# Kernel optimization log

Hardware: AMD Instinct MI355X
Metric: run time of the kernel (lower is better)

Reference implementation:

```python
import jax, jax.numpy as jnp
import numpy as np

C_REG = 0.1
MAX_ITER = 15
FEAT_SCALE = 0.05  # keep linear-kernel entries O(1) for a well-conditioned QP


def batched_kronecker(a, b):
    # a: (B,n,m), b: (B,p,q) -> (B, n*p, m*q); matches torch batched_kronecker
    B, n, m = a.shape
    _, p, q = b.shape
    return jnp.einsum('bij,bkl->bikjl', a, b).reshape(B, n * p, m * q)


def solve_qp_batch(G, e, h, A, b, max_iter):
    # Solves min_z 0.5 z^T G z + e^T z  s.t.  z <= h (C = I), A z = b
    # via a primal-dual interior-point method, batched over tasks.
    # (Same QP as qpth.QPFunction with C = identity.)
    def solve_one(G, e, h, A, b):
        nz = G.shape[0]
        neq = A.shape[0]
        nineq = h.shape[0]  # == nz since C = I
        z0 = jnp.zeros(nz, G.dtype)
        nu0 = jnp.zeros(neq, G.dtype)
        s0 = jnp.ones(nineq, G.dtype)
        lam0 = jnp.ones(nineq, G.dtype)

        def step(carry, _):
            z, nu, s, lam = carry
            rd = G @ z + e + lam + A.T @ nu          # dual residual (C^T lam = lam)
            rp = z + s - h                            # primal ineq residual (C z = z)
            rp2 = A @ z - b                           # primal eq residual
            mu = jnp.dot(s, lam) / nineq
            rc = lam * s - 0.1 * mu                   # centered complementarity
            d = lam / s
            H = G + jnp.diag(d)                       # G + C^T diag(lam/s) C with C = I
            r1 = -rd + (rc - lam * rp) / s
            KKT = jnp.block([[H, A.T], [A, jnp.zeros((neq, neq), G.dtype)]])
            rhs = jnp.concatenate([r1, -rp2])
            sol = jnp.linalg.solve(KKT, rhs)
            dz = sol[:nz]
            dnu = sol[nz:]
            ds = -rp - dz
            dlam = (-rc - lam * ds) / s
            a_s = jnp.min(jnp.where(ds < 0, -s / ds, jnp.inf))
            a_l = jnp.min(jnp.where(dlam < 0, -lam / dlam, jnp.inf))
            alpha = jnp.minimum(1.0, 0.99 * jnp.minimum(a_s, a_l))
            return (z + alpha * dz, nu + alpha * dnu, s + alpha * ds, lam + alpha * dlam), None

        (z, _, _, _), _ = jax.lax.scan(step, (z0, nu0, s0, lam0), None, length=max_iter)
        return z

    return jax.vmap(solve_one)(G, e, h, A, b)


def setup_inputs() -> dict:
    key = jax.random.key(0)
    k1, k2, k3 = jax.random.split(key, 3)
    B, N, K, Q, D = 32, 10, 10, 15, 512
    support = jax.random.normal(k1, (B, N, K, D), dtype=jnp.float32) * FEAT_SCALE
    support_labels = jax.random.randint(k2, (B, N, K), 0, N)
    query = jax.random.normal(k3, (B, N, Q, D), dtype=jnp.float32) * FEAT_SCALE
    return {"support": support, "support_labels": support_labels, "query": query}


def reference(support, support_labels, query):
    B, N, K, D = support.shape
    Q = query.shape[2]
    n_way = N
    n_support = N * K
    sup = support.reshape(B, n_support, D)
    qry = query.reshape(B, N * Q, D)

    # Gram matrix and block-kronecker QP Hessian: G = K(sup,sup) kron I_nway + I
    kernel = jnp.einsum('bnd,bmd->bnm', sup, sup)
    I_way = jnp.broadcast_to(jnp.eye(n_way, dtype=sup.dtype), (B, n_way, n_way))
    G = batched_kronecker(kernel, I_way) + jnp.eye(n_way * n_support, dtype=sup.dtype)

    y = jax.nn.one_hot(support_labels.reshape(B, n_support), n_way, dtype=sup.dtype)
    y_flat = y.reshape(B, n_support * n_way)
    e = -y_flat
    h = C_REG * y_flat

    # A = I_nsupport kron ones(1, n_way): sums alphas over classes per support point
    I_sup = jnp.broadcast_to(jnp.eye(n_support, dtype=sup.dtype), (B, n_support, n_support))
    A = batched_kronecker(I_sup, jnp.ones((B, 1, n_way), dtype=sup.dtype))
    b = jnp.zeros((B, n_support), dtype=sup.dtype)

    qp_sol = solve_qp_batch(G, e, h, A, b, MAX_ITER)  # (B, n_support*n_way)

    compat = jnp.einsum('bnd,bmd->bnm', sup, qry)     # (B, n_support, n_query)
    qp_sol = qp_sol.reshape(B, n_support, n_way)
    logits = jnp.einsum('bsq,bsn->bqn', compat, qp_sol)  # (B, n_query, n_way)
    return logits
```

## Files before the change

### kernel.cpp

```cpp
#include <hip/hip_runtime.h>

constexpr int kB   = 32;
constexpr int kNS  = 100;
constexpr int kNW  = 10;
constexpr int kNZ  = 1000;
constexpr int kD   = 512;
constexpr int kNQ  = 150;
constexpr int kIt  = 15;
constexpr int kPan = 4;
constexpr int kGrp = 8;
constexpr int kRQ  = 13;
constexpr int kNSP = kGrp * kRQ;

__global__ __launch_bounds__(128) void gram_kernel(const float* __restrict__ sup,
                                                   float* __restrict__ Kf)
{
    const int i = blockIdx.x;
    const int b = blockIdx.y;
    const int tid = threadIdx.x;
    __shared__ float rowi[kD];
    const float* supb = sup + (size_t)b * kNS * kD;
    reinterpret_cast<float4*>(rowi)[tid] =
        reinterpret_cast<const float4*>(supb + (size_t)i * kD)[tid];
    __syncthreads();
    for (int j = tid; j < kNS; j += 128) {
        const float4* rj = reinterpret_cast<const float4*>(supb + (size_t)j * kD);
        float acc = 0.0f;
        for (int d4 = 0; d4 < kD / 4; ++d4) {
            float4 v = rj[d4];
            acc += rowi[4*d4+0]*v.x + rowi[4*d4+1]*v.y
                 + rowi[4*d4+2]*v.z + rowi[4*d4+3]*v.w;
        }
        Kf[((size_t)b * kNS + i) * kNS + j] = acc;
    }
}

__global__ __launch_bounds__(256) void compat_kernel(const float* __restrict__ sup,
                                                     const float* __restrict__ qry,
                                                     float* __restrict__ compat)
{
    const int i = blockIdx.x;
    const int b = blockIdx.y;
    const int tid = threadIdx.x;
    __shared__ float rowi[kD];
    const float* supb = sup + (size_t)b * kNS * kD;
    const float* qryb = qry + (size_t)b * kNQ * kD;
    if (tid < 128)
        reinterpret_cast<float4*>(rowi)[tid] =
            reinterpret_cast<const float4*>(supb + (size_t)i * kD)[tid];
    __syncthreads();
    for (int j = tid; j < kNQ; j += 256) {
        const float4* rj = reinterpret_cast<const float4*>(qryb + (size_t)j * kD);
        float acc = 0.0f;
        for (int d4 = 0; d4 < kD / 4; ++d4) {
            float4 v = rj[d4];
            acc += rowi[4*d4+0]*v.x + rowi[4*d4+1]*v.y
                 + rowi[4*d4+2]*v.z + rowi[4*d4+3]*v.w;
        }
        compat[((size_t)b * kNS + i) * kNQ + j] = acc;
    }
}

__global__ __launch_bounds__(256) void init_kernel(double* __restrict__ z,
                                                   double* __restrict__ nu,
                                                   double* __restrict__ s,
                                                   double* __restrict__ lam,
                                                   double* __restrict__ mu_g)
{
    const int b = blockIdx.x;
    const int tid = threadIdx.x;
    for (int m = tid; m < kNZ; m += 256) {
        z[b*kNZ + m]   = 0.0;
        s[b*kNZ + m]   = 1.0;
        lam[b*kNZ + m] = 1.0;
    }
    if (tid < kNS) nu[b*kNS + tid] = 0.0;
    if (tid == 0)  mu_g[b] = 1.0;
}

__device__ __forceinline__ void adj4_solvef(const float B[4][4],
                                            const float b1[4], const float b2[4],
                                            float m1[4], float m2[4])
{
    const float s0 = B[0][0]*B[1][1] - B[1][0]*B[0][1];
    const float s1 = B[0][0]*B[1][2] - B[1][0]*B[0][2];
    const float s2 = B[0][0]*B[1][3] - B[1][0]*B[0][3];
    const float s3 = B[0][1]*B[1][2] - B[1][1]*B[0][2];
    const float s4 = B[0][1]*B[1][3] - B[1][1]*B[0][3];
    const float s5 = B[0][2]*B[1][3] - B[1][2]*B[0][3];
    const float c5 = B[2][2]*B[3][3] - B[3][2]*B[2][3];
    const float c4 = B[2][1]*B[3][3] - B[3][1]*B[2][3];
    const float c3 = B[2][1]*B[3][2] - B[3][1]*B[2][2];
    const float c2 = B[2][0]*B[3][3] - B[3][0]*B[2][3];
    const float c1 = B[2][0]*B[3][2] - B[3][0]*B[2][2];
    const float c0 = B[2][0]*B[3][1] - B[3][0]*B[2][1];
    const float det = s0*c5 - s1*c4 + s2*c3 + s3*c2 - s4*c1 + s5*c0;
    const float id = 1.0f / det;
    {
        const float r0 = ( B[1][1]*c5 - B[1][2]*c4 + B[1][3]*c3) * id;
        const float r1 = (-B[0][1]*c5 + B[0][2]*c4 - B[0][3]*c3) * id;
        const float r2 = ( B[3][1]*s5 - B[3][2]*s4 + B[3][3]*s3) * id;
        const float r3 = (-B[2][1]*s5 + B[2][2]*s4 - B[2][3]*s3) * id;
        m1[0] = r0*b1[0] + r1*b1[1] + r2*b1[2] + r3*b1[3];
        m2[0] = r0*b2[0] + r1*b2[1] + r2*b2[2] + r3*b2[3];
    }
    {
        const float r0 = (-B[1][0]*c5 + B[1][2]*c2 - B[1][3]*c1) * id;
        const float r1 = ( B[0][0]*c5 - B[0][2]*c2 + B[0][3]*c1) * id;
        const float r2 = (-B[3][0]*s5 + B[3][2]*s2 - B[3][3]*s1) * id;
        const float r3 = ( B[2][0]*s5 - B[2][2]*s2 + B[2][3]*s1) * id;
        m1[1] = r0*b1[0] + r1*b1[1] + r2*b1[2] + r3*b1[3];
        m2[1] = r0*b2[0] + r1*b2[1] + r2*b2[2] + r3*b2[3];
    }
    {
        const float r0 = ( B[1][0]*c4 - B[1][1]*c2 + B[1][3]*c0) * id;
        const float r1 = (-B[0][0]*c4 + B[0][1]*c2 - B[0][3]*c0) * id;
        const float r2 = ( B[3][0]*s4 - B[3][1]*s2 + B[3][3]*s0) * id;
        const float r3 = (-B[2][0]*s4 + B[2][1]*s2 - B[2][3]*s0) * id;
        m1[2] = r0*b1[0] + r1*b1[1] + r2*b1[2] + r3*b1[3];
        m2[2] = r0*b2[0] + r1*b2[1] + r2*b2[2] + r3*b2[3];
    }
    {
        const float r0 = (-B[1][0]*c3 + B[1][1]*c1 - B[1][2]*c0) * id;
        const float r1 = ( B[0][0]*c3 - B[0][1]*c1 + B[0][2]*c0) * id;
        const float r2 = (-B[3][0]*s3 + B[3][1]*s1 - B[3][2]*s0) * id;
        const float r3 = ( B[2][0]*s3 - B[2][1]*s1 + B[2][2]*s0) * id;
        m1[3] = r0*b1[0] + r1*b1[1] + r2*b1[2] + r3*b1[3];
        m2[3] = r0*b2[0] + r1*b2[1] + r2*b2[2] + r3*b2[3];
    }
}

#define PANEL_UPDATE2F(H1, H2, WSG, BUF, BASE, SCL1, SCL2, M1, M2)            \
    {                                                                          \
        _Pragma("unroll")                                                      \
        for (int r = 0; r < kRQ; ++r) { H1[r] *= SCL1; H2[r] *= SCL2; }        \
        _Pragma("unroll")                                                      \
        for (int p = 0; p < kPan; ++p) {                                       \
            const float mp1 = M1[p], mp2 = M2[p];                              \
            float w[kRQ];                                                      \
            _Pragma("unroll")                                                  \
            for (int u = 0; u < kRQ; ++u) w[u] = WSG[BUF][p][BASE + u];        \
            __builtin_amdgcn_sched_barrier(0);                                 \
            _Pragma("unroll")                                                  \
            for (int u = 0; u < kRQ; ++u) {                                    \
                H1[u] = fmaf(-mp1, w[u], H1[u]);                               \
                H2[u] = fmaf(-mp2, w[u], H2[u]);                               \
            }                                                                  \
        }                                                                      \
    }

__global__ __launch_bounds__(512) void ipm_invert_kernel(
    const float* __restrict__ Kf, const int* __restrict__ labels,
    const double* __restrict__ z, const double* __restrict__ nu,
    const double* __restrict__ s, const double* __restrict__ lam,
    const double* __restrict__ mu_g,
    float* __restrict__ Hinv, double* __restrict__ tvec)
{
    const int b = blockIdx.x / kNW;
    const int a = blockIdx.x - b * kNW;
    const int tid = threadIdx.x;
    const int h = tid >> 6;
    const int lane = tid & 63;
    const int base = h * kRQ;
    const int j1 = lane;
    const int j2 = 64 + lane;
    const bool a2 = (j2 < kNS);
    const int js2 = a2 ? j2 : j1;

    __shared__ double za[kNS], sa[kNS], la[kNS], nus[kNS], r1s[kNS];
    __shared__ float  daf[kNS];
    __shared__ double part[kGrp][kNS];
    __shared__ alignas(16) float Wr [2][kPan][kNSP + 8];
    __shared__ alignas(16) float Wsg[2][kPan][kNSP + 8];
    __shared__ int labs[kNS];

    const double* zb = z   + (size_t)b * kNZ;
    const double* sb = s   + (size_t)b * kNZ;
    const double* lb = lam + (size_t)b * kNZ;
    const float*  Kb = Kf  + (size_t)b * kNS * kNS;

    if (tid < kNS) {
        double zv = zb[tid * kNW + a];
        double sv = sb[tid * kNW + a];
        double lv = lb[tid * kNW + a];
        za[tid] = zv; sa[tid] = sv; la[tid] = lv;
        daf[tid] = (float)(lv / sv);
        nus[tid]  = nu[b * kNS + tid];
        labs[tid] = labels[b * kNS + tid];
    }
    if (h == 0 && j2 >= kNS && j2 < kNSP) {
        #pragma unroll
        for (int bf = 0; bf < 2; ++bf)
            #pragma unroll
            for (int p = 0; p < kPan; ++p) { Wr[bf][p][j2] = 0.0f; Wsg[bf][p][j2] = 0.0f; }
    }
    __syncthreads();

    float h1[kRQ], h2[kRQ];
    double kz1 = 0.0, kz2 = 0.0;
    #pragma unroll
    for (int r = 0; r < kRQ; ++r) {
        const int i = base + r;
        if (i < kNS) {
            float kv1 = Kb[(size_t)i * kNS + j1];
            float kv2 = Kb[(size_t)i * kNS + js2];
            kz1 += (double)kv1 * za[i];
            kz2 += (double)kv2 * za[i];
            h1[r] = (i == j1)  ? (kv1 + 1.0f + daf[j1])  : kv1;
            h2[r] = (i == js2) ? (kv2 + 1.0f + daf[js2]) : kv2;
        } else { h1[r] = 0.0f; h2[r] = 0.0f; }
    }
    part[h][j1] = kz1;
    if (a2) part[h][j2] = kz2;
    if (h == 0) {
        #pragma unroll
        for (int p = 0; p < kPan; ++p) {
            Wr [0][p][j1] = h1[p];  Wsg[0][p][j1] = h1[p];
            if (a2) { Wr[0][p][j2] = h2[p]; Wsg[0][p][j2] = h2[p]; }
        }
    }
    __syncthreads();
    if (tid < kNS) {
        const double mu = mu_g[b];
        const int i = tid;
        double kz = 0.0;
        #pragma unroll
        for (int g = 0; g < kGrp; ++g) kz += part[g][i];
        double yv = (labs[i] == a) ? 1.0 : 0.0;
        double rd = kz + za[i] - yv + la[i] + nus[i];
        double rp = za[i] + sa[i] - 0.1 * yv;
        double rc = la[i] * sa[i] - 0.1 * mu;
        r1s[i] = -rd + (rc - la[i] * rp) / sa[i];
    }

    #pragma unroll 1
    for (int k0 = 0; k0 < kNS; k0 += kPan) {
        const int buf = (k0 >> 2) & 1, nbuf = 1 - buf;
        __syncthreads();
        float B[4][4];
        #pragma unroll
        for (int p = 0; p < 4; ++p)
            #pragma unroll
            for (int q = 0; q < 4; ++q)
                B[p][q] = Wr[buf][p][k0 + q];

        const bool inp1 = (j1 >= k0) && (j1 < k0 + kPan);
        const bool inp2 = (js2 >= k0) && (js2 < k0 + kPan);
        float b1[4], b2[4];
        #pragma unroll
        for (int p = 0; p < 4; ++p) {
            b1[p] = inp1 ? ((j1  - k0 == p) ? 1.0f : 0.0f) : Wr[buf][p][j1];
            b2[p] = inp2 ? ((js2 - k0 == p) ? 1.0f : 0.0f) : Wr[buf][p][js2];
        }
        float m1[4], m2[4];
        adj4_solvef(B, b1, b2, m1, m2);
        const float scl1 = inp1 ? 0.0f : 1.0f;
        const float scl2 = inp2 ? 0.0f : 1.0f;
        PANEL_UPDATE2F(h1, h2, Wsg, buf, base, scl1, scl2, m1, m2);

        if (k0 < base + kRQ && k0 + kPan - 1 >= base) {
            #pragma unroll
            for (int r = 0; r < kRQ; ++r) {
                const int i = base + r;
                if (i >= k0 && i < k0 + kPan) {
                    const int p = i - k0;
                    h1[r] = m1[p];
                    h2[r] = m2[p];
                }
            }
        }
        const int kn0 = k0 + kPan;
        if (kn0 < kNS && kn0 < base + kRQ && kn0 + kPan - 1 >= base) {
            #pragma unroll
            for (int r = 0; r < kRQ; ++r) {
                const int i = base + r;
                if (i >= kn0 && i < kn0 + kPan) {
                    const int p = i - kn0;
                    Wr [nbuf][p][j1] = h1[r];
                    Wsg[nbuf][p][j1] = (j1 < kn0) ? -h1[r] : h1[r];
                    if (a2) {
                        Wr [nbuf][p][j2] = h2[r];
                        Wsg[nbuf][p][j2] = (j2 < kn0) ? -h2[r] : h2[r];
                    }
                }
            }
        }
    }

    float* Hb = Hinv + (size_t)(b * kNW + a) * kNS * kNS;
    double tp1 = 0.0, tp2 = 0.0;
    #pragma unroll
    for (int r = 0; r < kRQ; ++r) {
        const int i = base + r;
        if (i < kNS) {
            Hb[(size_t)i * kNS + j1] = h1[r];
            tp1 += (double)h1[r] * r1s[i];
            if (a2) { Hb[(size_t)i * kNS + j2] = h2[r]; tp2 += (double)h2[r] * r1s[i]; }
        }
    }
    part[h][j1] = tp1;
    if (a2) part[h][j2] = tp2;
    __syncthreads();
    if (tid < kNS) {
        double t = 0.0;
        #pragma unroll
        for (int g = 0; g < kGrp; ++g) t += part[g][tid];
        tvec[(size_t)(b * kNW + a) * kNS + tid] = t;
    }
}

__global__ __launch_bounds__(256) void sbuild_kernel(const float* __restrict__ Hinv,
                                                     float* __restrict__ Sg)
{
    const int b  = blockIdx.x / kNW;
    const int rc = blockIdx.x - b * kNW;
    const int tid = threadIdx.x;
    const float* Hb = Hinv + (size_t)b * kNW * kNS * kNS;
    for (int e = tid; e < kNS * kNS / kNW; e += 256) {
        const int idx = rc * (kNS * kNS / kNW) + e;
        double acc = 0.0;
        #pragma unroll
        for (int a = 0; a < kNW; ++a) acc += (double)Hb[(size_t)a * kNS * kNS + idx];
        Sg[(size_t)b * kNS * kNS + idx] = (float)acc;
    }
}

__global__ __launch_bounds__(512) void schur_solve_kernel(
    const float* __restrict__ Sg, const double* __restrict__ tvec,
    const double* __restrict__ z, double* __restrict__ dnu_g)
{
    const int b = blockIdx.x;
    const int tid = threadIdx.x;
    const int h = tid >> 6;
    const int lane = tid & 63;
    const int base = h * kRQ;
    const int j1 = lane;
    const int j2 = 64 + lane;
    const bool a2 = (j2 <= kNS);
    const int js2 = a2 ? j2 : j1;

    __shared__ double rhs[kNS];
    __shared__ alignas(16) float Wr [2][kPan][kNSP + 8];
    __shared__ alignas(16) float Wsg[2][kPan][kNSP + 8];

    const float*  Sb = Sg   + (size_t)b * kNS * kNS;
    const double* tb = tvec + (size_t)b * kNW * kNS;
    const double* zb = z    + (size_t)b * kNZ;

    if (tid < kNS) {
        double acc = 0.0, rp2 = 0.0;
        #pragma unroll
        for (int a = 0; a < kNW; ++a) {
            acc += tb[a * kNS + tid];
            rp2 += zb[tid * kNW + a];
        }
        rhs[tid] = acc + rp2;
    }
    if (h == 0 && j2 > kNS && j2 < kNSP) {
        #pragma unroll
        for (int bf = 0; bf < 2; ++bf)
            #pragma unroll
            for (int p = 0; p < kPan; ++p) { Wr[bf][p][j2] = 0.0f; Wsg[bf][p][j2] = 0.0f; }
    }
    __syncthreads();

    float h1[kRQ], h2[kRQ];
    #pragma unroll
    for (int r = 0; r < kRQ; ++r) {
        const int i = base + r;
        if (i < kNS) {
            h1[r] = Sb[(size_t)i * kNS + j1];
            h2[r] = (js2 == kNS) ? (float)rhs[i]
                  : Sb[(size_t)i * kNS + ((js2 < kNS) ? js2 : 0)];
        } else { h1[r] = 0.0f; h2[r] = 0.0f; }
    }
    if (h == 0) {
        #pragma unroll
        for (int p = 0; p < kPan; ++p) {
            Wr [0][p][j1] = h1[p];  Wsg[0][p][j1] = h1[p];
            if (a2) { Wr[0][p][j2] = h2[p]; Wsg[0][p][j2] = h2[p]; }
        }
    }

    #pragma unroll 1
    for (int k0 = 0; k0 < kNS; k0 += kPan) {
        const int buf = (k0 >> 2) & 1, nbuf = 1 - buf;
        __syncthreads();
        float B[4][4];
        #pragma unroll
        for (int p = 0; p < 4; ++p)
            #pragma unroll
            for (int q = 0; q < 4; ++q)
                B[p][q] = Wr[buf][p][k0 + q];

        const bool inp1 = (j1 >= k0) && (j1 < k0 + kPan);
        const bool inp2 = (js2 >= k0) && (js2 < k0 + kPan);
        float b1[4], b2[4];
        #pragma unroll
        for (int p = 0; p < 4; ++p) {
            b1[p] = inp1 ? ((j1  - k0 == p) ? 1.0f : 0.0f) : Wr[buf][p][j1];
            b2[p] = inp2 ? ((js2 - k0 == p) ? 1.0f : 0.0f) : Wr[buf][p][js2];
        }
        float m1[4], m2[4];
        adj4_solvef(B, b1, b2, m1, m2);
        const float scl1 = inp1 ? 0.0f : 1.0f;
        const float scl2 = inp2 ? 0.0f : 1.0f;
        PANEL_UPDATE2F(h1, h2, Wsg, buf, base, scl1, scl2, m1, m2);

        if (k0 < base + kRQ && k0 + kPan - 1 >= base) {
            #pragma unroll
            for (int r = 0; r < kRQ; ++r) {
                const int i = base + r;
                if (i >= k0 && i < k0 + kPan) {
                    const int p = i - k0;
                    h1[r] = m1[p];
                    h2[r] = m2[p];
                }
            }
        }
        const int kn0 = k0 + kPan;
        if (kn0 < kNS && kn0 < base + kRQ && kn0 + kPan - 1 >= base) {
            #pragma unroll
            for (int r = 0; r < kRQ; ++r) {
                const int i = base + r;
                if (i >= kn0 && i < kn0 + kPan) {
                    const int p = i - kn0;
                    Wr [nbuf][p][j1] = h1[r];
                    Wsg[nbuf][p][j1] = (j1 < kn0) ? -h1[r] : h1[r];
                    if (a2) {
                        Wr [nbuf][p][j2] = h2[r];
                        Wsg[nbuf][p][j2] = (j2 < kn0) ? -h2[r] : h2[r];
                    }
                }
            }
        }
    }

    if (j2 == kNS) {
        #pragma unroll
        for (int r = 0; r < kRQ; ++r) {
            const int i = base + r;
            if (i < kNS) dnu_g[(size_t)b * kNS + i] = (double)h2[r];
        }
    }
}

__global__ __launch_bounds__(512) void dz_kernel(
    const int* __restrict__ labels,
    const float* __restrict__ Hinv, const double* __restrict__ tvec,
    const double* __restrict__ dnu_g,
    const double* __restrict__ z, const double* __restrict__ s,
    const double* __restrict__ lam, const double* __restrict__ mu_g,
    double* __restrict__ dz_g, double* __restrict__ ds_g,
    double* __restrict__ dl_g, double* __restrict__ minr_g)
{
    const int b = blockIdx.x / kNW;
    const int a = blockIdx.x - b * kNW;
    const int tid = threadIdx.x;
    const int h = tid >> 7;
    const int j = tid & 127;

    __shared__ double dnus[kNS];
    __shared__ double p4[4][kNS];
    __shared__ double red[512];

    const float* Hb = Hinv + (size_t)(b * kNW + a) * kNS * kNS;

    if (tid < kNS) dnus[tid] = dnu_g[(size_t)b * kNS + tid];
    __syncthreads();

    if (j < kNS) {
        double p = 0.0;
        #pragma unroll
        for (int r = 0; r < kNS / 4; ++r)
            p += (double)Hb[(size_t)(h * (kNS / 4) + r) * kNS + j] * dnus[h * (kNS / 4) + r];
        p4[h][j] = p;
    }
    __syncthreads();

    double lmin = 1e300;
    if (tid < kNS) {
        const int i = tid;
        const size_t m = (size_t)b * kNZ + i * kNW + a;
        const double mu = mu_g[b];
        double dz = tvec[(size_t)(b * kNW + a) * kNS + i]
                  - (p4[0][i] + p4[1][i] + p4[2][i] + p4[3][i]);
        double yv = (labels[b * kNS + i] == a) ? 1.0 : 0.0;
        double zv = z[m], sv = s[m], lv = lam[m];
        double rp = zv + sv - 0.1 * yv;
        double rc = lv * sv - 0.1 * mu;
        double ds = -rp - dz;
        double dl = (-rc - lv * ds) / sv;
        dz_g[m] = dz; ds_g[m] = ds; dl_g[m] = dl;
        if (ds < 0.0) lmin = fmin(lmin, -sv / ds);
        if (dl < 0.0) lmin = fmin(lmin, -lv / dl);
    }
    red[tid] = lmin; __syncthreads();
    for (int off = 256; off > 0; off >>= 1) {
        if (tid < off) red[tid] = fmin(red[tid], red[tid + off]);
        __syncthreads();
    }
    if (tid == 0) minr_g[b * kNW + a] = red[0];
}

__global__ __launch_bounds__(256) void update_kernel(
    const double* __restrict__ minr_g, const double* __restrict__ dnu_g,
    const double* __restrict__ dz_g, const double* __restrict__ ds_g,
    const double* __restrict__ dl_g,
    double* __restrict__ z, double* __restrict__ nu,
    double* __restrict__ s, double* __restrict__ lam,
    double* __restrict__ mu_g)
{
    const int b = blockIdx.x;
    const int tid = threadIdx.x;
    __shared__ double red[256];

    double am = 1e300;
    #pragma unroll
    for (int a = 0; a < kNW; ++a) am = fmin(am, minr_g[b * kNW + a]);
    const double alpha = fmin(1.0, 0.99 * am);

    double* zb = z   + (size_t)b * kNZ;
    double* sb = s   + (size_t)b * kNZ;
    double* lb = lam + (size_t)b * kNZ;

    double md = 0.0;
    #pragma unroll
    for (int tcl = 0; tcl < 4; ++tcl) {
        const int  e = tid + tcl * 256;
        const size_t m = (size_t)b * kNZ + e;
        if (e < kNZ) {
            double zn = zb[e] + alpha * dz_g[m];
            double sn = sb[e] + alpha * ds_g[m];
            double ln = lb[e] + alpha * dl_g[m];
            zb[e] = zn; sb[e] = sn; lb[e] = ln;
            md += sn * ln;
        }
    }
    red[tid] = md; __syncthreads();
    for (int off = 128; off > 0; off >>= 1) {
        if (tid < off) red[tid] += red[tid + off];
        __syncthreads();
    }
    if (tid == 0) mu_g[b] = red[0] / kNZ;
    if (tid < kNS) nu[(size_t)b * kNS + tid] += alpha * dnu_g[(size_t)b * kNS + tid];
}

__global__ __launch_bounds__(256) void logits_kernel(const float* __restrict__ compat,
                                                     const double* __restrict__ z,
                                                     float* __restrict__ out)
{
    const int b = blockIdx.x;
    const int tid = threadIdx.x;
    const float* cb = compat + (size_t)b * kNS * kNQ;
    const double* zb = z + (size_t)b * kNZ;
    __shared__ double zs[kNZ];
    for (int m = tid; m < kNZ; m += 256) zs[m] = zb[m];
    __syncthreads();
    for (int idx = tid; idx < kNQ * kNW; idx += 256) {
        int q = idx / kNW, n = idx - q * kNW;
        double acc = 0.0;
        for (int s2 = 0; s2 < kNS; ++s2)
            acc += (double)cb[(size_t)s2 * kNQ + q] * zs[s2 * kNW + n];
        out[(size_t)b * kNQ * kNW + idx] = (float)acc;
    }
}

extern "C" void kernel_launch(void* const* d_in, const int* in_sizes, int n_in,
                              void* d_out, int out_size, void* d_ws, size_t ws_size,
                              hipStream_t stream)
{
    const float* sup    = (const float*)d_in[0];
    const int*   labels = (const int*)  d_in[1];
    const float* qry    = (const float*)d_in[2];
    float* out = (float*)d_out;

    char* ws = (char*)d_ws;
    size_t off = 0;
    auto alloc = [&](size_t bytes) -> void* {
        void* p = ws + off;
        off += (bytes + 255) & ~(size_t)255;
        return p;
    };
    float*  Kf     = (float*) alloc(sizeof(float)  * kB * kNS * kNS);
    double* z      = (double*)alloc(sizeof(double) * kB * kNZ);
    double* nu     = (double*)alloc(sizeof(double) * kB * kNS);
    double* s      = (double*)alloc(sizeof(double) * kB * kNZ);
    double* lam    = (double*)alloc(sizeof(double) * kB * kNZ);
    double* mu_g   = (double*)alloc(sizeof(double) * kB);
    float*  Hinv   = (float*) alloc(sizeof(float)  * kB * kNW * kNS * kNS);
    float*  Sg     = (float*) alloc(sizeof(float)  * kB * kNS * kNS);
    double* tvec   = (double*)alloc(sizeof(double) * kB * kNW * kNS);
    double* dnu_g  = (double*)alloc(sizeof(double) * kB * kNS);
    double* dz_g   = (double*)alloc(sizeof(double) * kB * kNZ);
    double* ds_g   = (double*)alloc(sizeof(double) * kB * kNZ);
    double* dl_g   = (double*)alloc(sizeof(double) * kB * kNZ);
    double* minr_g = (double*)alloc(sizeof(double) * kB * kNW);
    float*  compat = (float*) alloc(sizeof(float)  * kB * kNS * kNQ);

    gram_kernel  <<<dim3(kNS, kB), 128, 0, stream>>>(sup, Kf);
    compat_kernel<<<dim3(kNS, kB), 256, 0, stream>>>(sup, qry, compat);
    init_kernel  <<<kB, 256, 0, stream>>>(z, nu, s, lam, mu_g);

    for (int it = 0; it < kIt; ++it) {
        ipm_invert_kernel<<<kB * kNW, 512, 0, stream>>>(Kf, labels, z, nu, s,
                                                        lam, mu_g, Hinv, tvec);
        sbuild_kernel<<<kB * kNW, 256, 0, stream>>>(Hinv, Sg);
        schur_solve_kernel<<<kB, 512, 0, stream>>>(Sg, tvec, z, dnu_g);
        dz_kernel<<<kB * kNW, 512, 0, stream>>>(labels, Hinv, tvec, dnu_g,
                                                z, s, lam, mu_g,
                                                dz_g, ds_g, dl_g, minr_g);
        update_kernel<<<kB, 256, 0, stream>>>(minr_g, dnu_g, dz_g, ds_g, dl_g,
                                              z, nu, s, lam, mu_g);
    }

    logits_kernel<<<kB, 256, 0, stream>>>(compat, z, out);
}
```

Baseline: 2.653 ms.

## Fuse IPM update into next iteration and drop separate Schur-sum kernel

Removes the update_kernel by having each ipm_invert block apply the previous step (alpha from per-class minima, mu from a quadratic in alpha built from partial sums) to its own slice, with ping-pong nu buffers; logits applies the final step. Removes sbuild_kernel by summing the ten Hinv blocks directly while loading the Schur matrix in schur_solve. Merges the gram and compat kernels into one wave-per-row dot-product kernel. This cuts the number of launches per iteration from five to three and the round trips through global memory. In exchange, schur_solve does more strided global reads on a single block per task, and mu is now computed algebraically instead of from the updated vectors, which can round slightly differently.

```diff
diff --git a/kernel.cpp b/kernel.cpp
--- a/kernel.cpp
+++ b/kernel.cpp
@@ -12,52 +12,44 @@
 constexpr int kRQ  = 13;
 constexpr int kNSP = kGrp * kRQ;
 
-__global__ __launch_bounds__(128) void gram_kernel(const float* __restrict__ sup,
-                                                   float* __restrict__ Kf)
-{
-    const int i = blockIdx.x;
-    const int b = blockIdx.y;
-    const int tid = threadIdx.x;
-    __shared__ float rowi[kD];
-    const float* supb = sup + (size_t)b * kNS * kD;
-    reinterpret_cast<float4*>(rowi)[tid] =
-        reinterpret_cast<const float4*>(supb + (size_t)i * kD)[tid];
-    __syncthreads();
-    for (int j = tid; j < kNS; j += 128) {
-        const float4* rj = reinterpret_cast<const float4*>(supb + (size_t)j * kD);
-        float acc = 0.0f;
-        for (int d4 = 0; d4 < kD / 4; ++d4) {
-            float4 v = rj[d4];
-            acc += rowi[4*d4+0]*v.x + rowi[4*d4+1]*v.y
-                 + rowi[4*d4+2]*v.z + rowi[4*d4+3]*v.w;
-        }
-        Kf[((size_t)b * kNS + i) * kNS + j] = acc;
-    }
-}
-
-__global__ __launch_bounds__(256) void compat_kernel(const float* __restrict__ sup,
-                                                     const float* __restrict__ qry,
-                                                     float* __restrict__ compat)
-{
-    const int i = blockIdx.x;
-    const int b = blockIdx.y;
-    const int tid = threadIdx.x;
-    __shared__ float rowi[kD];
+__global__ __launch_bounds__(256) void gemm_kernel(const float* __restrict__ sup,
+                                                   const float* __restrict__ qry,
+                                                   float* __restrict__ Kf,
+                                                   float* __restrict__ compat)
+{
+    const int i0 = blockIdx.x * 2;
+    const int b  = blockIdx.y;
+    const int w    = threadIdx.x >> 6;
+    const int lane = threadIdx.x & 63;
     const float* supb = sup + (size_t)b * kNS * kD;
     const float* qryb = qry + (size_t)b * kNQ * kD;
-    if (tid < 128)
-        reinterpret_cast<float4*>(rowi)[tid] =
-            reinterpret_cast<const float4*>(supb + (size_t)i * kD)[tid];
-    __syncthreads();
-    for (int j = tid; j < kNQ; j += 256) {
-        const float4* rj = reinterpret_cast<const float4*>(qryb + (size_t)j * kD);
-        float acc = 0.0f;
-        for (int d4 = 0; d4 < kD / 4; ++d4) {
-            float4 v = rj[d4];
-            acc += rowi[4*d4+0]*v.x + rowi[4*d4+1]*v.y
-                 + rowi[4*d4+2]*v.z + rowi[4*d4+3]*v.w;
-        }
-        compat[((size_t)b * kNS + i) * kNQ + j] = acc;
+    const float4* r0 = reinterpret_cast<const float4*>(supb + (size_t)i0 * kD) + 2 * lane;
+    const float4* r1 = reinterpret_cast<const float4*>(supb + (size_t)(i0 + 1) * kD) + 2 * lane;
+    const float4 a0 = r0[0], a1 = r0[1];
+    const float4 q0 = r1[0], q1 = r1[1];
+    for (int t = w; t < kNS + kNQ; t += 4) {
+        const float* rowt = (t < kNS) ? (supb + (size_t)t * kD)
+                                      : (qryb + (size_t)(t - kNS) * kD);
+        const float4* rt = reinterpret_cast<const float4*>(rowt) + 2 * lane;
+        const float4 v0 = rt[0], v1 = rt[1];
+        float pa = a0.x*v0.x + a0.y*v0.y + a0.z*v0.z + a0.w*v0.w
+                 + a1.x*v1.x + a1.y*v1.y + a1.z*v1.z + a1.w*v1.w;
+        float pb = q0.x*v0.x + q0.y*v0.y + q0.z*v0.z + q0.w*v0.w
+                 + q1.x*v1.x + q1.y*v1.y + q1.z*v1.z + q1.w*v1.w;
+        #pragma unroll
+        for (int msk = 1; msk < 64; msk <<= 1) {
+            pa += __shfl_xor(pa, msk);
+            pb += __shfl_xor(pb, msk);
+        }
+        if (lane == 0) {
+            if (t < kNS) {
+                Kf[((size_t)b * kNS + i0    ) * kNS + t] = pa;
+                Kf[((size_t)b * kNS + i0 + 1) * kNS + t] = pb;
+            } else {
+                compat[((size_t)b * kNS + i0    ) * kNQ + (t - kNS)] = pa;
+                compat[((size_t)b * kNS + i0 + 1) * kNQ + (t - kNS)] = pb;
+            }
+        }
     }
 }
 
@@ -151,10 +143,13 @@
 
 __global__ __launch_bounds__(512) void ipm_invert_kernel(
     const float* __restrict__ Kf, const int* __restrict__ labels,
-    const double* __restrict__ z, const double* __restrict__ nu,
-    const double* __restrict__ s, const double* __restrict__ lam,
-    const double* __restrict__ mu_g,
-    float* __restrict__ Hinv, double* __restrict__ tvec)
+    double* __restrict__ z, double* __restrict__ s, double* __restrict__ lam,
+    const double* __restrict__ nu_in, double* __restrict__ nu_out,
+    const double* __restrict__ dnu_g, const double* __restrict__ dz_g,
+    const double* __restrict__ ds_g, const double* __restrict__ dl_g,
+    const double* __restrict__ minr_g, const double* __restrict__ part3_g,
+    double* __restrict__ mu_g,
+    float* __restrict__ Hinv, double* __restrict__ tvec, const int first)
 {
     const int b = blockIdx.x / kNW;
     const int a = blockIdx.x - b * kNW;
@@ -174,18 +169,39 @@
     __shared__ alignas(16) float Wsg[2][kPan][kNSP + 8];
     __shared__ int labs[kNS];
 
-    const double* zb = z   + (size_t)b * kNZ;
-    const double* sb = s   + (size_t)b * kNZ;
-    const double* lb = lam + (size_t)b * kNZ;
-    const float*  Kb = Kf  + (size_t)b * kNS * kNS;
-
+    const float* Kb = Kf + (size_t)b * kNS * kNS;
+
+    double mu = 1.0;
     if (tid < kNS) {
-        double zv = zb[tid * kNW + a];
-        double sv = sb[tid * kNW + a];
-        double lv = lb[tid * kNW + a];
+        double alpha = 0.0;
+        if (!first) {
+            double am = 1e300;
+            #pragma unroll
+            for (int aa = 0; aa < kNW; ++aa) am = fmin(am, minr_g[b * kNW + aa]);
+            alpha = fmin(1.0, 0.99 * am);
+            double P0 = 0.0, P1 = 0.0, P2 = 0.0;
+            #pragma unroll
+            for (int aa = 0; aa < kNW; ++aa) {
+                const double* pp = part3_g + (size_t)(b * kNW + aa) * 3;
+                P0 += pp[0]; P1 += pp[1]; P2 += pp[2];
+            }
+            mu = (P0 + alpha * (P1 + alpha * P2)) / kNZ;
+        }
+        const size_t m = (size_t)b * kNZ + tid * kNW + a;
+        double zv = z[m], sv = s[m], lv = lam[m];
+        double nv = nu_in[b * kNS + tid];
+        if (!first) {
+            zv += alpha * dz_g[m]; sv += alpha * ds_g[m]; lv += alpha * dl_g[m];
+            z[m] = zv; s[m] = sv; lam[m] = lv;
+            nv += alpha * dnu_g[b * kNS + tid];
+        }
+        if (a == 0) {
+            nu_out[b * kNS + tid] = nv;
+            if (tid == 0) mu_g[b] = mu;
+        }
         za[tid] = zv; sa[tid] = sv; la[tid] = lv;
         daf[tid] = (float)(lv / sv);
-        nus[tid]  = nu[b * kNS + tid];
+        nus[tid] = nv;
         labs[tid] = labels[b * kNS + tid];
     }
     if (h == 0 && j2 >= kNS && j2 < kNSP) {
@@ -221,7 +237,6 @@
     }
     __syncthreads();
     if (tid < kNS) {
-        const double mu = mu_g[b];
         const int i = tid;
         double kz = 0.0;
         #pragma unroll
@@ -309,24 +324,8 @@
     }
 }
 
-__global__ __launch_bounds__(256) void sbuild_kernel(const float* __restrict__ Hinv,
-                                                     float* __restrict__ Sg)
-{
-    const int b  = blockIdx.x / kNW;
-    const int rc = blockIdx.x - b * kNW;
-    const int tid = threadIdx.x;
-    const float* Hb = Hinv + (size_t)b * kNW * kNS * kNS;
-    for (int e = tid; e < kNS * kNS / kNW; e += 256) {
-        const int idx = rc * (kNS * kNS / kNW) + e;
-        double acc = 0.0;
-        #pragma unroll
-        for (int a = 0; a < kNW; ++a) acc += (double)Hb[(size_t)a * kNS * kNS + idx];
-        Sg[(size_t)b * kNS * kNS + idx] = (float)acc;
-    }
-}
-
 __global__ __launch_bounds__(512) void schur_solve_kernel(
-    const float* __restrict__ Sg, const double* __restrict__ tvec,
+    const float* __restrict__ Hinv, const double* __restrict__ tvec,
     const double* __restrict__ z, double* __restrict__ dnu_g)
 {
     const int b = blockIdx.x;
@@ -343,7 +342,7 @@
     __shared__ alignas(16) float Wr [2][kPan][kNSP + 8];
     __shared__ alignas(16) float Wsg[2][kPan][kNSP + 8];
 
-    const float*  Sb = Sg   + (size_t)b * kNS * kNS;
+    const float*  Hbase = Hinv + (size_t)b * kNW * kNS * kNS;
     const double* tb = tvec + (size_t)b * kNW * kNS;
     const double* zb = z    + (size_t)b * kNZ;
 
@@ -369,9 +368,15 @@
     for (int r = 0; r < kRQ; ++r) {
         const int i = base + r;
         if (i < kNS) {
-            h1[r] = Sb[(size_t)i * kNS + j1];
-            h2[r] = (js2 == kNS) ? (float)rhs[i]
-                  : Sb[(size_t)i * kNS + ((js2 < kNS) ? js2 : 0)];
+            double acc1 = 0.0, acc2 = 0.0;
+            #pragma unroll
+            for (int a = 0; a < kNW; ++a) {
+                const float* Ha = Hbase + ((size_t)a * kNS + i) * kNS;
+                acc1 += (double)Ha[j1];
+                if (js2 < kNS) acc2 += (double)Ha[js2];
+            }
+            h1[r] = (float)acc1;
+            h2[r] = (js2 == kNS) ? (float)rhs[i] : (float)acc2;
         } else { h1[r] = 0.0f; h2[r] = 0.0f; }
     }
     if (h == 0) {
@@ -452,7 +457,8 @@
     const double* __restrict__ z, const double* __restrict__ s,
     const double* __restrict__ lam, const double* __restrict__ mu_g,
     double* __restrict__ dz_g, double* __restrict__ ds_g,
-    double* __restrict__ dl_g, double* __restrict__ minr_g)
+    double* __restrict__ dl_g, double* __restrict__ minr_g,
+    double* __restrict__ part3_g)
 {
     const int b = blockIdx.x / kNW;
     const int a = blockIdx.x - b * kNW;
@@ -462,7 +468,7 @@
 
     __shared__ double dnus[kNS];
     __shared__ double p4[4][kNS];
-    __shared__ double red[512];
+    __shared__ double red[512], rA[512], rB[512], rC[512];
 
     const float* Hb = Hinv + (size_t)(b * kNW + a) * kNS * kNS;
 
@@ -478,7 +484,7 @@
     }
     __syncthreads();
 
-    double lmin = 1e300;
+    double lmin = 1e300, p0 = 0.0, p1 = 0.0, p2 = 0.0;
     if (tid < kNS) {
         const int i = tid;
         const size_t m = (size_t)b * kNZ + i * kNW + a;
@@ -494,60 +500,32 @@
         dz_g[m] = dz; ds_g[m] = ds; dl_g[m] = dl;
         if (ds < 0.0) lmin = fmin(lmin, -sv / ds);
         if (dl < 0.0) lmin = fmin(lmin, -lv / dl);
-    }
-    red[tid] = lmin; __syncthreads();
+        p0 = sv * lv;
+        p1 = sv * dl + lv * ds;
+        p2 = ds * dl;
+    }
+    red[tid] = lmin; rA[tid] = p0; rB[tid] = p1; rC[tid] = p2;
+    __syncthreads();
     for (int off = 256; off > 0; off >>= 1) {
-        if (tid < off) red[tid] = fmin(red[tid], red[tid + off]);
+        if (tid < off) {
+            red[tid] = fmin(red[tid], red[tid + off]);
+            rA[tid] += rA[tid + off];
+            rB[tid] += rB[tid + off];
+            rC[tid] += rC[tid + off];
+        }
         __syncthreads();
     }
-    if (tid == 0) minr_g[b * kNW + a] = red[0];
-}
-
-__global__ __launch_bounds__(256) void update_kernel(
-    const double* __restrict__ minr_g, const double* __restrict__ dnu_g,
-    const double* __restrict__ dz_g, const double* __restrict__ ds_g,
-    const double* __restrict__ dl_g,
-    double* __restrict__ z, double* __restrict__ nu,
-    double* __restrict__ s, double* __restrict__ lam,
-    double* __restrict__ mu_g)
-{
-    const int b = blockIdx.x;
-    const int tid = threadIdx.x;
-    __shared__ double red[256];
-
-    double am = 1e300;
-    #pragma unroll
-    for (int a = 0; a < kNW; ++a) am = fmin(am, minr_g[b * kNW + a]);
-    const double alpha = fmin(1.0, 0.99 * am);
-
-    double* zb = z   + (size_t)b * kNZ;
-    double* sb = s   + (size_t)b * kNZ;
-    double* lb = lam + (size_t)b * kNZ;
-
-    double md = 0.0;
-    #pragma unroll
-    for (int tcl = 0; tcl < 4; ++tcl) {
-        const int  e = tid + tcl * 256;
-        const size_t m = (size_t)b * kNZ + e;
-        if (e < kNZ) {
-            double zn = zb[e] + alpha * dz_g[m];
-            double sn = sb[e] + alpha * ds_g[m];
-            double ln = lb[e] + alpha * dl_g[m];
-            zb[e] = zn; sb[e] = sn; lb[e] = ln;
-            md += sn * ln;
-        }
-    }
-    red[tid] = md; __syncthreads();
-    for (int off = 128; off > 0; off >>= 1) {
-        if (tid < off) red[tid] += red[tid + off];
-        __syncthreads();
-    }
-    if (tid == 0) mu_g[b] = red[0] / kNZ;
-    if (tid < kNS) nu[(size_t)b * kNS + tid] += alpha * dnu_g[(size_t)b * kNS + tid];
+    if (tid == 0) {
+        minr_g[b * kNW + a] = red[0];
+        double* pp = part3_g + (size_t)(b * kNW + a) * 3;
+        pp[0] = rA[0]; pp[1] = rB[0]; pp[2] = rC[0];
+    }
 }
 
 __global__ __launch_bounds__(256) void logits_kernel(const float* __restrict__ compat,
                                                      const double* __restrict__ z,
+                                                     const double* __restrict__ dz_g,
+                                                     const double* __restrict__ minr_g,
                                                      float* __restrict__ out)
 {
     const int b = blockIdx.x;
@@ -555,7 +533,12 @@
     const float* cb = compat + (size_t)b * kNS * kNQ;
     const double* zb = z + (size_t)b * kNZ;
     __shared__ double zs[kNZ];
-    for (int m = tid; m < kNZ; m += 256) zs[m] = zb[m];
+    double am = 1e300;
+    #pragma unroll
+    for (int aa = 0; aa < kNW; ++aa) am = fmin(am, minr_g[b * kNW + aa]);
+    const double alpha = fmin(1.0, 0.99 * am);
+    for (int m = tid; m < kNZ; m += 256)
+        zs[m] = zb[m] + alpha * dz_g[(size_t)b * kNZ + m];
     __syncthreads();
     for (int idx = tid; idx < kNQ * kNW; idx += 256) {
         int q = idx / kNW, n = idx - q * kNW;
@@ -584,35 +567,36 @@
     };
     float*  Kf     = (float*) alloc(sizeof(float)  * kB * kNS * kNS);
     double* z      = (double*)alloc(sizeof(double) * kB * kNZ);
-    double* nu     = (double*)alloc(sizeof(double) * kB * kNS);
+    double* nuA    = (double*)alloc(sizeof(double) * kB * kNS);
+    double* nuB    = (double*)alloc(sizeof(double) * kB * kNS);
     double* s      = (double*)alloc(sizeof(double) * kB * kNZ);
     double* lam    = (double*)alloc(sizeof(double) * kB * kNZ);
     double* mu_g   = (double*)alloc(sizeof(double) * kB);
     float*  Hinv   = (float*) alloc(sizeof(float)  * kB * kNW * kNS * kNS);
-    float*  Sg     = (float*) alloc(sizeof(float)  * kB * kNS * kNS);
     double* tvec   = (double*)alloc(sizeof(double) * kB * kNW * kNS);
     double* dnu_g  = (double*)alloc(sizeof(double) * kB * kNS);
     double* dz_g   = (double*)alloc(sizeof(double) * kB * kNZ);
     double* ds_g   = (double*)alloc(sizeof(double) * kB * kNZ);
     double* dl_g   = (double*)alloc(sizeof(double) * kB * kNZ);
     double* minr_g = (double*)alloc(sizeof(double) * kB * kNW);
+    double* part3_g= (double*)alloc(sizeof(double) * kB * kNW * 3);
     float*  compat = (float*) alloc(sizeof(float)  * kB * kNS * kNQ);
 
-    gram_kernel  <<<dim3(kNS, kB), 128, 0, stream>>>(sup, Kf);
-    compat_kernel<<<dim3(kNS, kB), 256, 0, stream>>>(sup, qry, compat);
-    init_kernel  <<<kB, 256, 0, stream>>>(z, nu, s, lam, mu_g);
+    gemm_kernel<<<dim3(kNS / 2, kB), 256, 0, stream>>>(sup, qry, Kf, compat);
+    init_kernel<<<kB, 256, 0, stream>>>(z, nuA, s, lam, mu_g);
 
     for (int it = 0; it < kIt; ++it) {
-        ipm_invert_kernel<<<kB * kNW, 512, 0, stream>>>(Kf, labels, z, nu, s,
-                                                        lam, mu_g, Hinv, tvec);
-        sbuild_kernel<<<kB * kNW, 256, 0, stream>>>(Hinv, Sg);
-        schur_solve_kernel<<<kB, 512, 0, stream>>>(Sg, tvec, z, dnu_g);
+        const double* nu_in  = (it & 1) ? nuB : nuA;
+        double*       nu_out = (it & 1) ? nuA : nuB;
+        ipm_invert_kernel<<<kB * kNW, 512, 0, stream>>>(
+            Kf, labels, z, s, lam, nu_in, nu_out,
+            dnu_g, dz_g, ds_g, dl_g, minr_g, part3_g, mu_g,
+            Hinv, tvec, (it == 0) ? 1 : 0);
+        schur_solve_kernel<<<kB, 512, 0, stream>>>(Hinv, tvec, z, dnu_g);
         dz_kernel<<<kB * kNW, 512, 0, stream>>>(labels, Hinv, tvec, dnu_g,
                                                 z, s, lam, mu_g,
-                                                dz_g, ds_g, dl_g, minr_g);
-        update_kernel<<<kB, 256, 0, stream>>>(minr_g, dnu_g, dz_g, ds_g, dl_g,
-                                              z, nu, s, lam, mu_g);
-    }
-
-    logits_kernel<<<kB, 256, 0, stream>>>(compat, z, out);
-}
+                                                dz_g, ds_g, dl_g, minr_g, part3_g);
+    }
+
+    logits_kernel<<<kB, 256, 0, stream>>>(compat, z, dz_g, minr_g, out);
+}
```

New measurement: 2.966 ms. +11.8%, slower.
